# Optimization experiments

Hardware: AMD Instinct MI355X
Metric: run time of the kernel (lower is better)

The kernel has to match this reference:

```python
import jax, jax.numpy as jnp
import numpy as np

NUM_USERS = 50000
NUM_ITEMS = 20000
N_NODES = NUM_USERS + NUM_ITEMS
D = 128
CONTENT_DIM = 512
BATCH = 8192
N_EDGES = 500000
NEG_SLOPE = 0.2  # GATConv leaky_relu slope


def setup_inputs() -> dict:
    key = jax.random.key(0)
    ks = jax.random.split(key, 16)
    return {
        "user_ids": jax.random.randint(ks[0], (BATCH,), 0, NUM_USERS),
        "item_ids": jax.random.randint(ks[1], (BATCH,), 0, NUM_ITEMS),
        "content_features": jax.random.normal(ks[2], (BATCH, CONTENT_DIM), jnp.float32),
        "edge_index": jax.random.randint(ks[3], (2, N_EDGES), 0, N_NODES),
        "user_emb_w": jax.random.normal(ks[4], (NUM_USERS, D), jnp.float32) * 0.05,
        "item_emb_w": jax.random.normal(ks[5], (NUM_ITEMS, D), jnp.float32) * 0.05,
        "content_proj_w": jax.random.normal(ks[6], (D, CONTENT_DIM), jnp.float32) * 0.04,
        "content_proj_b": jnp.zeros((D,), jnp.float32),
        "conv1_lin_w": jax.random.normal(ks[7], (2 * D, 2 * D), jnp.float32) * 0.06,
        "conv1_att_src": jax.random.normal(ks[8], (2, D), jnp.float32) * 0.1,
        "conv1_att_dst": jax.random.normal(ks[9], (2, D), jnp.float32) * 0.1,
        "conv1_bias": jnp.zeros((2 * D,), jnp.float32),
        "conv2_lin_w": jax.random.normal(ks[10], (D, 2 * D), jnp.float32) * 0.06,
        "conv2_att_src": jax.random.normal(ks[11], (1, D), jnp.float32) * 0.1,
        "conv2_att_dst": jax.random.normal(ks[12], (1, D), jnp.float32) * 0.1,
        "conv2_bias": jnp.zeros((D,), jnp.float32),
        "pred_w1": jax.random.normal(ks[13], (D, 3 * D), jnp.float32) * 0.05,
        "pred_b1": jnp.zeros((D,), jnp.float32),
        "pred_w2": jax.random.normal(ks[14], (1, D), jnp.float32) * 0.09,
        "pred_b2": jnp.zeros((1,), jnp.float32),
    }


def gat_conv(x, src, dst, lin_w, att_src, att_dst, bias, heads, out_ch):
    # PyG GATConv (shared lin for src/dst, concat=True, add_self_loops handled outside)
    n = x.shape[0]
    h = (x @ lin_w.T).reshape(n, heads, out_ch)          # [N,H,C]
    a_src = jnp.sum(h * att_src, axis=-1)                # [N,H]
    a_dst = jnp.sum(h * att_dst, axis=-1)                # [N,H]
    alpha = jax.nn.leaky_relu(a_src[src] + a_dst[dst], NEG_SLOPE)  # [E,H]
    # softmax over incoming edges of each destination node
    amax = jax.ops.segment_max(alpha, dst, num_segments=n)
    ex = jnp.exp(alpha - amax[dst])
    denom = jax.ops.segment_sum(ex, dst, num_segments=n)
    w = ex / denom[dst]                                  # [E,H]
    out = jax.ops.segment_sum(h[src] * w[:, :, None], dst, num_segments=n)
    return out.reshape(n, heads * out_ch) + bias


def _forward(user_ids, item_ids, edge_index, content_features, user_emb_w, item_emb_w,
             content_proj_w, content_proj_b, conv1_lin_w, conv1_att_src, conv1_att_dst,
             conv1_bias, conv2_lin_w, conv2_att_src, conv2_att_dst, conv2_bias,
             pred_w1, pred_b1, pred_w2, pred_b2):
    u_emb = user_emb_w[user_ids]                         # [B,D]
    i_emb = item_emb_w[item_ids]                         # [B,D]
    c_emb = content_features @ content_proj_w.T + content_proj_b  # [B,D]
    # scatter-init sparse node features (only batch nodes are nonzero, as in source)
    x = jnp.zeros((N_NODES, 2 * D), jnp.float32)
    x = x.at[user_ids].set(jnp.concatenate([u_emb, jnp.zeros_like(c_emb)], axis=1))
    x = x.at[NUM_USERS + item_ids].set(jnp.concatenate([i_emb, c_emb], axis=1))
    # add self loops (fill_value irrelevant: edge_weight unused by GATConv)
    loops = jnp.arange(N_NODES, dtype=edge_index.dtype)
    src = jnp.concatenate([edge_index[0], loops])
    dst = jnp.concatenate([edge_index[1], loops])
    x = jax.nn.elu(gat_conv(x, src, dst, conv1_lin_w, conv1_att_src, conv1_att_dst, conv1_bias, 2, D))
    # dropout inactive (eval mode)
    x = gat_conv(x, src, dst, conv2_lin_w, conv2_att_src, conv2_att_dst, conv2_bias, 1, D)
    combined = jnp.concatenate([u_emb, x[NUM_USERS + item_ids], x[user_ids]], axis=1)  # [B,3D]
    h = jax.nn.relu(combined @ pred_w1.T + pred_b1)
    return (h @ pred_w2.T + pred_b2).squeeze(-1)         # [B]


def reference(user_ids, item_ids, content_features, edge_index, user_emb_w, item_emb_w,
              content_proj_w, content_proj_b, conv1_lin_w, conv1_att_src, conv1_att_dst,
              conv1_bias, conv2_lin_w, conv2_att_src, conv2_att_dst, conv2_bias,
              pred_w1, pred_b1, pred_w2, pred_b2):
    return _forward(user_ids, item_ids, edge_index, content_features, user_emb_w, item_emb_w,
                    content_proj_w, content_proj_b, conv1_lin_w, conv1_att_src, conv1_att_dst,
                    conv1_bias, conv2_lin_w, conv2_att_src, conv2_att_dst, conv2_bias,
                    pred_w1, pred_b1, pred_w2, pred_b2)
```

## Files before the change

### kernel.cpp

```cpp
#include <hip/hip_runtime.h>
#include <hip/hip_bf16.h>

#define NU 50000
#define NI 20000
#define NN 70000
#define DD 128
#define BB 8192
#define EE 500000
#define ET 570000
#define NTASK 16384

__device__ __forceinline__ float lrelu(float x) { return x > 0.f ? x : 0.2f * x; }

typedef __attribute__((ext_vector_type(8))) short bf16x8;
typedef __attribute__((ext_vector_type(8))) unsigned short u16x8;
typedef __attribute__((ext_vector_type(4))) float f32x4;

__device__ __forceinline__ unsigned short f2bf_rne(float f) {
  unsigned int u = __builtin_bit_cast(unsigned int, f);
  u += 0x7FFFu + ((u >> 16) & 1u);
  return (unsigned short)(u >> 16);
}
__device__ __forceinline__ float bf2f(unsigned short h) {
  unsigned int u = ((unsigned int)h) << 16;
  return __builtin_bit_cast(float, u);
}

__global__ __launch_bounds__(256) void clear_kernel(
    unsigned int* __restrict__ wsw,
    unsigned int offA, unsigned int nA,
    unsigned int offB, unsigned int nB,
    unsigned int offC, unsigned int nC,
    float* __restrict__ out) {
  unsigned int idx = blockIdx.x * 256 + threadIdx.x;
  unsigned int stride = gridDim.x * 256;
  for (unsigned int i = idx; i < nA; i += stride) wsw[offA + i] = 0xFFFFFFFFu;
  for (unsigned int i = idx; i < nB; i += stride) wsw[offB + i] = 0u;
  for (unsigned int i = idx; i < nC; i += stride) wsw[offC + i] = 0u;
  for (unsigned int i = idx; i < BB; i += stride) out[i] = 0.f;
}

template <int GATHER, int MODE>
__device__ __forceinline__ void gemm_core(
    int bm, int bn,
    const float* __restrict__ A,
    const unsigned short* __restrict__ Bh, const unsigned short* __restrict__ Bl,
    const float* __restrict__ bias, float* __restrict__ C,
    unsigned short* __restrict__ Cb, int ldc,
    int M, int N, int K, int act,
    const int* __restrict__ idx0, const int* __restrict__ idx1,
    const int* __restrict__ mapv,
    const float* __restrict__ gA0, const float* __restrict__ gA1,
    const float* __restrict__ att_s, const float* __restrict__ att_d,
    float* __restrict__ a1s, float* __restrict__ a1d) {
  __shared__ __align__(16) unsigned short sAh[8][64][8];
  __shared__ __align__(16) unsigned short sAl[8][64][8];
  __shared__ __align__(16) unsigned short sBh[8][64][8];
  __shared__ __align__(16) unsigned short sBl[8][64][8];
  int tid = threadIdx.x;
  int lane = tid & 63, w = tid >> 6;
  int wr = (w >> 1) * 32, wc = (w & 1) * 32;
  int fr = lane & 15, fk = lane >> 4;
  f32x4 acc[2][2] = {};

  for (int k0 = 0; k0 < K; k0 += 64) {
    __syncthreads();
#pragma unroll
    for (int t = 0; t < 2; t++) {
      int f = tid + t * 256;
      int row = f >> 3, kb = f & 7;
      int kg = k0 + kb * 8;
      const float* ap;
      if (GATHER == 1) {
        int sec = kg >> 7;
        int kc = kg & 127;
        int r = bm + row;
        if (sec == 0)      ap = &gA0[(size_t)idx0[r] * 128 + kc];
        else if (sec == 1) ap = &gA1[(size_t)mapv[NU + idx1[r]] * 128 + kc];
        else               ap = &gA1[(size_t)mapv[idx0[r]] * 128 + kc];
      } else if (GATHER == 2) {
        ap = &gA0[(size_t)idx0[bm + row] * K + kg];
      } else {
        ap = &A[(size_t)(bm + row) * K + kg];
      }
      float4 v0 = *reinterpret_cast<const float4*>(ap);
      float4 v1 = *reinterpret_cast<const float4*>(ap + 4);
      float vv[8] = {v0.x, v0.y, v0.z, v0.w, v1.x, v1.y, v1.z, v1.w};
      u16x8 hv, lv;
#pragma unroll
      for (int j = 0; j < 8; j++) {
        unsigned short hh = f2bf_rne(vv[j]);
        hv[j] = hh;
        lv[j] = (unsigned short)(__builtin_bit_cast(unsigned int, vv[j] - bf2f(hh)) >> 16);
      }
      *reinterpret_cast<u16x8*>(&sAh[kb][row][0]) = hv;
      *reinterpret_cast<u16x8*>(&sAl[kb][row][0]) = lv;
    }
#pragma unroll
    for (int t = 0; t < 2; t++) {
      int f = tid + t * 256;
      int row = f >> 3, kb = f & 7;
      int kg = k0 + kb * 8;
      *reinterpret_cast<u16x8*>(&sBh[kb][row][0]) =
          *reinterpret_cast<const u16x8*>(&Bh[(size_t)(bn + row) * K + kg]);
      *reinterpret_cast<u16x8*>(&sBl[kb][row][0]) =
          *reinterpret_cast<const u16x8*>(&Bl[(size_t)(bn + row) * K + kg]);
    }
    __syncthreads();
#pragma unroll
    for (int s = 0; s < 2; s++) {
      int kb = s * 4 + fk;
      bf16x8 ah0 = *reinterpret_cast<const bf16x8*>(&sAh[kb][wr + fr][0]);
      bf16x8 ah1 = *reinterpret_cast<const bf16x8*>(&sAh[kb][wr + 16 + fr][0]);
      bf16x8 al0 = *reinterpret_cast<const bf16x8*>(&sAl[kb][wr + fr][0]);
      bf16x8 al1 = *reinterpret_cast<const bf16x8*>(&sAl[kb][wr + 16 + fr][0]);
      bf16x8 bh0 = *reinterpret_cast<const bf16x8*>(&sBh[kb][wc + fr][0]);
      bf16x8 bh1 = *reinterpret_cast<const bf16x8*>(&sBh[kb][wc + 16 + fr][0]);
      bf16x8 bl0 = *reinterpret_cast<const bf16x8*>(&sBl[kb][wc + fr][0]);
      bf16x8 bl1 = *reinterpret_cast<const bf16x8*>(&sBl[kb][wc + 16 + fr][0]);
      acc[0][0] = __builtin_amdgcn_mfma_f32_16x16x32_bf16(al0, bh0, acc[0][0], 0, 0, 0);
      acc[0][0] = __builtin_amdgcn_mfma_f32_16x16x32_bf16(ah0, bl0, acc[0][0], 0, 0, 0);
      acc[0][0] = __builtin_amdgcn_mfma_f32_16x16x32_bf16(ah0, bh0, acc[0][0], 0, 0, 0);
      acc[0][1] = __builtin_amdgcn_mfma_f32_16x16x32_bf16(al0, bh1, acc[0][1], 0, 0, 0);
      acc[0][1] = __builtin_amdgcn_mfma_f32_16x16x32_bf16(ah0, bl1, acc[0][1], 0, 0, 0);
      acc[0][1] = __builtin_amdgcn_mfma_f32_16x16x32_bf16(ah0, bh1, acc[0][1], 0, 0, 0);
      acc[1][0] = __builtin_amdgcn_mfma_f32_16x16x32_bf16(al1, bh0, acc[1][0], 0, 0, 0);
      acc[1][0] = __builtin_amdgcn_mfma_f32_16x16x32_bf16(ah1, bl0, acc[1][0], 0, 0, 0);
      acc[1][0] = __builtin_amdgcn_mfma_f32_16x16x32_bf16(ah1, bh0, acc[1][0], 0, 0, 0);
      acc[1][1] = __builtin_amdgcn_mfma_f32_16x16x32_bf16(al1, bh1, acc[1][1], 0, 0, 0);
      acc[1][1] = __builtin_amdgcn_mfma_f32_16x16x32_bf16(ah1, bl1, acc[1][1], 0, 0, 0);
      acc[1][1] = __builtin_amdgcn_mfma_f32_16x16x32_bf16(ah1, bh1, acc[1][1], 0, 0, 0);
    }
  }
  if (MODE == 1) {
    int head = bn >> 7;
    float ps[2][4] = {{0.f}}, pd[2][4] = {{0.f}};
#pragma unroll
    for (int j = 0; j < 2; j++) {
      int col = bn + wc + j * 16 + fr;
      float asc = att_s[col], adc = att_d[col];
#pragma unroll
      for (int i = 0; i < 2; i++) {
#pragma unroll
        for (int r = 0; r < 4; r++) {
          float v = acc[i][j][r];
          ps[i][r] += v * asc;
          pd[i][r] += v * adc;
          Cb[(size_t)(bm + wr + i * 16 + fk * 4 + r) * ldc + col] = f2bf_rne(v);
        }
      }
    }
#pragma unroll
    for (int o = 1; o < 16; o <<= 1) {
#pragma unroll
      for (int i = 0; i < 2; i++)
#pragma unroll
        for (int r = 0; r < 4; r++) {
          ps[i][r] += __shfl_xor(ps[i][r], o);
          pd[i][r] += __shfl_xor(pd[i][r], o);
        }
    }
    if (fr == 0) {
#pragma unroll
      for (int i = 0; i < 2; i++) {
#pragma unroll
        for (int r = 0; r < 4; r++) {
          int t = bm + wr + i * 16 + fk * 4 + r;
          int v = (t < BB) ? idx0[t] : NU + idx1[t - BB];
          if (mapv[v] == t) {
            atomicAdd(&a1s[(size_t)v * 2 + head], ps[i][r]);
            atomicAdd(&a1d[(size_t)v * 2 + head], pd[i][r]);
          }
        }
      }
    }
    return;
  }
  if (MODE == 2) {
    float part[2][4] = {{0.f}};
#pragma unroll
    for (int j = 0; j < 2; j++) {
      int col = bn + wc + j * 16 + fr;
      float bj = bias[col];
      float wv = att_s[col];
#pragma unroll
      for (int i = 0; i < 2; i++) {
#pragma unroll
        for (int r = 0; r < 4; r++) {
          float v = fmaxf(acc[i][j][r] + bj, 0.f);
          part[i][r] += v * wv;
        }
      }
    }
#pragma unroll
    for (int o = 1; o < 16; o <<= 1) {
#pragma unroll
      for (int i = 0; i < 2; i++)
#pragma unroll
        for (int r = 0; r < 4; r++) part[i][r] += __shfl_xor(part[i][r], o);
    }
    if (fr == 0) {
#pragma unroll
      for (int i = 0; i < 2; i++) {
#pragma unroll
        for (int r = 0; r < 4; r++) {
          int row = bm + wr + i * 16 + fk * 4 + r;
          float add = part[i][r];
          if (bn == 0 && wc == 0) add += att_d[0];
          atomicAdd(&a1s[row], add);
        }
      }
    }
    return;
  }
#pragma unroll
  for (int j = 0; j < 2; j++) {
    int col = bn + wc + j * 16 + fr;
    float bj = bias ? bias[col] : 0.f;
#pragma unroll
    for (int i = 0; i < 2; i++) {
#pragma unroll
      for (int r = 0; r < 4; r++) {
        int row = bm + wr + i * 16 + fk * 4 + r;
        float v = acc[i][j][r] + bj;
        if (act == 1) v = fmaxf(v, 0.f);
        C[(size_t)row * ldc + col] = v;
      }
    }
  }
}

template <int GATHER, int MODE>
__global__ __launch_bounds__(256) void gemm_mfma(
    const float* __restrict__ A,
    const unsigned short* __restrict__ Bh, const unsigned short* __restrict__ Bl,
    const float* __restrict__ bias, float* __restrict__ C,
    unsigned short* __restrict__ Cb, int ldc,
    int M, int N, int K, int act,
    const int* __restrict__ idx0, const int* __restrict__ idx1,
    const int* __restrict__ mapv,
    const float* __restrict__ gA0, const float* __restrict__ gA1,
    const float* __restrict__ att_s, const float* __restrict__ att_d,
    float* __restrict__ a1s, float* __restrict__ a1d) {
  gemm_core<GATHER, MODE>(blockIdx.x * 64, blockIdx.y * 64,
                          A, Bh, Bl, bias, C, Cb, ldc, M, N, K, act,
                          idx0, idx1, mapv, gA0, gA1, att_s, att_d, a1s, a1d);
}

#define GEMMB 256
__global__ __launch_bounds__(256) void cembfill_kernel(
    const unsigned short* __restrict__ wch, const unsigned short* __restrict__ wcl,
    const float* __restrict__ bc, float* __restrict__ XaC,
    const int* __restrict__ widx, const float* __restrict__ content,
    const int* __restrict__ ei, int* __restrict__ fill, int* __restrict__ col,
    const int* __restrict__ mapv, unsigned char* __restrict__ needed) {
  int bid = blockIdx.x;
  if (bid < GEMMB) {
    gemm_core<2, 0>((bid >> 1) * 64, (bid & 1) * 64,
                    nullptr, wch, wcl, bc, XaC, nullptr, 256,
                    BB, DD, 512, 0, widx, nullptr, nullptr, content, nullptr,
                    nullptr, nullptr, nullptr, nullptr);
    return;
  }
  int e = (bid - GEMMB) * 256 + threadIdx.x;
  if (e >= ET) return;
  int src, dst;
  if (e < EE) { src = ei[e]; dst = ei[EE + e]; }
  else { src = e - EE; dst = src; }
  int pos = atomicAdd(&fill[dst], 1);
  col[pos] = src;
  if (mapv[dst] >= 0) needed[src] = 1;
}

#define EB 2227
#define SPLB 832
#define XAB 4096
__global__ __launch_bounds__(256) void setup_kernel(
    const int* __restrict__ ei, const int* __restrict__ uid, const int* __restrict__ iid,
    int* __restrict__ deg, int* __restrict__ winner,
    const float* __restrict__ wc, unsigned short* wch, unsigned short* wcl,
    const float* __restrict__ w1, unsigned short* w1h, unsigned short* w1l,
    const float* __restrict__ w2, unsigned short* w2h, unsigned short* w2l,
    const float* __restrict__ pw1, unsigned short* p1h, unsigned short* p1l,
    const float* __restrict__ uemb, const float* __restrict__ iemb,
    float* __restrict__ Xa, int* __restrict__ map) {
  int bid = blockIdx.x, tid = threadIdx.x;
  if (bid < EB) {
    int e = bid * 256 + tid;
    if (e < BB) atomicMax(&winner[iid[e]], e);
    if (e >= ET) return;
    int dst = (e < EE) ? ei[EE + e] : (e - EE);
    atomicAdd(&deg[dst], 1);
    return;
  }
  if (bid < EB + SPLB) {
    int i = (bid - EB) * 256 + tid;
    const float* w; unsigned short* h; unsigned short* l; int idx;
    if (i < 65536) { w = wc; h = wch; l = wcl; idx = i; }
    else if (i < 131072) { w = w1; h = w1h; l = w1l; idx = i - 65536; }
    else if (i < 163840) { w = w2; h = w2h; l = w2l; idx = i - 131072; }
    else { w = pw1; h = p1h; l = p1l; idx = i - 163840; }
    float f = w[idx];
    unsigned short hh = f2bf_rne(f);
    h[idx] = hh;
    l[idx] = (unsigned short)(__builtin_bit_cast(unsigned int, f - bf2f(hh)) >> 16);
    return;
  }
  int t = (bid - EB - SPLB) * 4 + (tid >> 6);
  int lane = tid & 63;
  int c4 = lane * 4;
  if (t < BB) {
    int u = uid[t];
    float4 v = make_float4(0.f, 0.f, 0.f, 0.f);
    if (c4 < DD) v = *reinterpret_cast<const float4*>(&uemb[(size_t)u * DD + c4]);
    *reinterpret_cast<float4*>(&Xa[(size_t)t * 256 + c4]) = v;
    if (lane == 0) map[u] = t;
  } else {
    int it = iid[t - BB];
    if (c4 < DD) {
      float4 v = *reinterpret_cast<const float4*>(&iemb[(size_t)it * DD + c4]);
      *reinterpret_cast<float4*>(&Xa[(size_t)t * 256 + c4]) = v;
    }
    if (lane == 0) map[NU + it] = t;
  }
}

__global__ void rowstart_kernel(const int* __restrict__ deg, const int* __restrict__ winner,
                                const int* __restrict__ iid,
                                int* __restrict__ rowstart, int* __restrict__ fill,
                                int* __restrict__ counter, int* __restrict__ widx,
                                const float* __restrict__ w2,
                                const float* __restrict__ att2s, const float* __restrict__ att2d,
                                float* __restrict__ qs, float* __restrict__ qd) {
  int blk = blockIdx.x;
  if (blk == (NN + 255) / 256) {
    int k = threadIdx.x;
    float s = 0.f, d = 0.f;
#pragma unroll 4
    for (int j = 0; j < DD; j++) {
      float w = w2[(size_t)j * 256 + k];
      s += att2s[j] * w;
      d += att2d[j] * w;
    }
    qs[k] = s;
    qd[k] = d;
    return;
  }
  int v = blk * 256 + threadIdx.x;
  if (v < BB) widx[v] = winner[iid[v]];
  int lane = threadIdx.x & 63;
  int dv = (v < NN) ? deg[v] : 0;
  int x = dv;
#pragma unroll
  for (int o = 1; o < 64; o <<= 1) {
    int y = __shfl_up(x, o);
    if (lane >= o) x += y;
  }
  int tot = __shfl(x, 63);
  int base = 0;
  if (lane == 63) base = atomicAdd(counter, tot);
  base = __shfl(base, 63);
  if (v < NN) {
    int s = base + x - dv;
    rowstart[v] = s;
    fill[v] = s;
  }
}

__global__ __launch_bounds__(256) void conv1_agg_kernel(
    const int* __restrict__ col, const int* __restrict__ rowstart,
    const int* __restrict__ deg, const unsigned short* __restrict__ Hb,
    const int* __restrict__ map, const unsigned char* __restrict__ needed,
    const float* __restrict__ a1s, const float* __restrict__ a1d,
    const float* __restrict__ bias,
    const float* __restrict__ qs, const float* __restrict__ qd,
    unsigned short* __restrict__ x1b, float* __restrict__ a2s, float* __restrict__ a2d) {
  int v = blockIdx.x * 4 + (threadIdx.x >> 6);
  int lane = threadIdx.x & 63;
  if (!needed[v]) return;
  int head = lane >> 5;
  int d = deg[v], s0 = rowstart[v];
  float2 adv = *reinterpret_cast<const float2*>(&a1d[(size_t)v * 2]);
  float4 acc = make_float4(0.f, 0.f, 0.f, 0.f);
  float den0 = 0.f, den1 = 0.f;
  const unsigned short* hb = Hb + (lane << 2);
  for (int c0 = 0; c0 < d; c0 += 64) {
    int i = c0 + lane;
    bool act = i < d;
    int ci = act ? col[s0 + i] : 0;
    float2 asv = make_float2(0.f, 0.f);
    int ri = -1;
    if (act) {
      asv = *reinterpret_cast<const float2*>(&a1s[(size_t)ci * 2]);
      ri = map[ci];
    }
    float ex0 = act ? __expf(lrelu(asv.x + adv.x)) : 0.f;
    float ex1 = act ? __expf(lrelu(asv.y + adv.y)) : 0.f;
    den0 += ex0;
    den1 += ex1;
    unsigned long long msk = __ballot(act && ri >= 0);
    while (msk) {
      int s = __ffsll((unsigned long long)msk) - 1;
      msk &= msk - 1;
      int r = __shfl(ri, s);
      float e0 = __shfl(ex0, s), e1 = __shfl(ex1, s);
      float ex = head ? e1 : e0;
      ushort4 hv = *reinterpret_cast<const ushort4*>(&hb[(size_t)r << 8]);
      acc.x += ex * bf2f(hv.x); acc.y += ex * bf2f(hv.y);
      acc.z += ex * bf2f(hv.z); acc.w += ex * bf2f(hv.w);
    }
  }
#pragma unroll
  for (int o = 1; o < 64; o <<= 1) {
    den0 += __shfl_xor(den0, o);
    den1 += __shfl_xor(den1, o);
  }
  float inv = 1.f / (head ? den1 : den0);
  float4 b4 = *reinterpret_cast<const float4*>(&bias[lane << 2]);
  float4 o;
  o.x = fmaf(acc.x, inv, b4.x);
  o.y = fmaf(acc.y, inv, b4.y);
  o.z = fmaf(acc.z, inv, b4.z);
  o.w = fmaf(acc.w, inv, b4.w);
  o.x = o.x > 0.f ? o.x : __expf(o.x) - 1.f;
  o.y = o.y > 0.f ? o.y : __expf(o.y) - 1.f;
  o.z = o.z > 0.f ? o.z : __expf(o.z) - 1.f;
  o.w = o.w > 0.f ? o.w : __expf(o.w) - 1.f;
  ushort4 st;
  st.x = f2bf_rne(o.x); st.y = f2bf_rne(o.y);
  st.z = f2bf_rne(o.z); st.w = f2bf_rne(o.w);
  *reinterpret_cast<ushort4*>(&x1b[((size_t)v << 8) + (lane << 2)]) = st;
  float4 sv = *reinterpret_cast<const float4*>(&qs[lane << 2]);
  float4 dv = *reinterpret_cast<const float4*>(&qd[lane << 2]);
  float ps = o.x * sv.x + o.y * sv.y + o.z * sv.z + o.w * sv.w;
  float pd = o.x * dv.x + o.y * dv.y + o.z * dv.z + o.w * dv.w;
#pragma unroll
  for (int of = 1; of < 64; of <<= 1) { ps += __shfl_xor(ps, of); pd += __shfl_xor(pd, of); }
  if (lane == 0) { a2s[v] = ps; a2d[v] = pd; }
}

__global__ __launch_bounds__(256) void conv2_agg_kernel(
    const int* __restrict__ uid, const int* __restrict__ iid,
    const int* __restrict__ col, const int* __restrict__ rowstart,
    const int* __restrict__ deg, const int* __restrict__ map,
    const unsigned short* __restrict__ x1b,
    const float* __restrict__ a2s, const float* __restrict__ a2d,
    float* __restrict__ agg) {
  int t = blockIdx.x * 4 + (threadIdx.x >> 6);
  int lane = threadIdx.x & 63;
  int v = (t < BB) ? uid[t] : NU + iid[t - BB];
  if (map[v] != t) return;
  int d = deg[v], s0 = rowstart[v];
  float ad = a2d[v];
  float4 acc = make_float4(0.f, 0.f, 0.f, 0.f);
  float den = 0.f;
  const unsigned short* xb = x1b + (lane << 2);
  for (int c0 = 0; c0 < d; c0 += 64) {
    int i = c0 + lane;
    bool act = i < d;
    int ci = act ? col[s0 + i] : 0;
    float as = act ? a2s[ci] : 0.f;
    float ex = act ? __expf(lrelu(as + ad)) : 0.f;
    den += ex;
    int n = min(64, d - c0);
#pragma unroll 2
    for (int i2 = 0; i2 < n; i2++) {
      int r = __shfl(ci, i2);
      float e = __shfl(ex, i2);
      ushort4 hv = *reinterpret_cast<const ushort4*>(&xb[(size_t)r << 8]);
      acc.x += e * bf2f(hv.x); acc.y += e * bf2f(hv.y);
      acc.z += e * bf2f(hv.z); acc.w += e * bf2f(hv.w);
    }
  }
#pragma unroll
  for (int o = 1; o < 64; o <<= 1) den += __shfl_xor(den, o);
  float inv = 1.f / den;
  float4 o = make_float4(acc.x * inv, acc.y * inv, acc.z * inv, acc.w * inv);
  *reinterpret_cast<float4*>(&agg[((size_t)t << 8) + (lane << 2)]) = o;
}

extern "C" void kernel_launch(void* const* d_in, const int* in_sizes, int n_in,
                              void* d_out, int out_size, void* d_ws, size_t ws_size,
                              hipStream_t stream) {
  const int* uid = (const int*)d_in[0];
  const int* iid = (const int*)d_in[1];
  const float* content = (const float*)d_in[2];
  const int* ei = (const int*)d_in[3];
  const float* uemb = (const float*)d_in[4];
  const float* iemb = (const float*)d_in[5];
  const float* wc = (const float*)d_in[6];
  const float* bc = (const float*)d_in[7];
  const float* w1 = (const float*)d_in[8];
  const float* att1s = (const float*)d_in[9];
  const float* att1d = (const float*)d_in[10];
  const float* b1 = (const float*)d_in[11];
  const float* w2 = (const float*)d_in[12];
  const float* att2s = (const float*)d_in[13];
  const float* att2d = (const float*)d_in[14];
  const float* b2c = (const float*)d_in[15];
  const float* pw1 = (const float*)d_in[16];
  const float* pb1 = (const float*)d_in[17];
  const float* pw2 = (const float*)d_in[18];
  const float* pb2 = (const float*)d_in[19];
  float* out = (float*)d_out;
  char* ws = (char*)d_ws;

  size_t off = 0;
  auto alloc = [&](size_t bytes) {
    size_t o = off;
    off += (bytes + 255) & ~(size_t)255;
    return o;
  };
  size_t o_winner  = alloc(NI * 4);
  size_t o_map     = alloc(NN * 4);
  size_t o_a1s     = alloc((size_t)NN * 2 * 4);
  size_t o_a1d     = alloc((size_t)NN * 2 * 4);
  size_t o_deg     = alloc(NN * 4);
  size_t o_rs      = alloc(NN * 4);
  size_t o_fill    = alloc(NN * 4);
  size_t o_cnt     = alloc(4);
  size_t o_needed  = alloc(NN);
  size_t o_col     = alloc((size_t)ET * 4);
  size_t o_a2s     = alloc(NN * 4);
  size_t o_a2d     = alloc(NN * 4);
  size_t o_qs      = alloc(256 * 4);
  size_t o_qd      = alloc(256 * 4);
  size_t o_widx    = alloc(BB * 4);
  size_t o_wch = alloc(65536 * 2),  o_wcl = alloc(65536 * 2);
  size_t o_w1h = alloc(65536 * 2),  o_w1l = alloc(65536 * 2);
  size_t o_w2h = alloc(32768 * 2),  o_w2l = alloc(32768 * 2);
  size_t o_p1h = alloc(49152 * 2),  o_p1l = alloc(49152 * 2);
  size_t o_r1    = alloc(16777216 + 8388608);
  size_t o_xa    = o_r1;
  size_t o_hb    = o_r1 + 16777216;
  size_t o_agg   = o_r1;
  size_t o_out2c = o_r1 + 16777216;
  size_t o_x1b   = alloc((size_t)NN * 256 * 2);
  (void)ws_size; (void)in_sizes; (void)n_in; (void)out_size;

  int*   winner = (int*)(ws + o_winner);
  int*   map    = (int*)(ws + o_map);
  float* a1s    = (float*)(ws + o_a1s);
  float* a1d    = (float*)(ws + o_a1d);
  int*   deg    = (int*)(ws + o_deg);
  int*   rs     = (int*)(ws + o_rs);
  int*   fill   = (int*)(ws + o_fill);
  int*   cnt    = (int*)(ws + o_cnt);
  unsigned char* needed = (unsigned char*)(ws + o_needed);
  int*   col    = (int*)(ws + o_col);
  float* a2s    = (float*)(ws + o_a2s);
  float* a2d    = (float*)(ws + o_a2d);
  float* qs     = (float*)(ws + o_qs);
  float* qd     = (float*)(ws + o_qd);
  int*   widx   = (int*)(ws + o_widx);
  unsigned short* wch = (unsigned short*)(ws + o_wch);
  unsigned short* wcl = (unsigned short*)(ws + o_wcl);
  unsigned short* w1h = (unsigned short*)(ws + o_w1h);
  unsigned short* w1l = (unsigned short*)(ws + o_w1l);
  unsigned short* w2h = (unsigned short*)(ws + o_w2h);
  unsigned short* w2l = (unsigned short*)(ws + o_w2l);
  unsigned short* p1h = (unsigned short*)(ws + o_p1h);
  unsigned short* p1l = (unsigned short*)(ws + o_p1l);
  float* Xa     = (float*)(ws + o_xa);
  unsigned short* Hb = (unsigned short*)(ws + o_hb);
  float* agg    = (float*)(ws + o_agg);
  float* out2c  = (float*)(ws + o_out2c);
  unsigned short* x1b = (unsigned short*)(ws + o_x1b);

  {
    unsigned int offA = (unsigned int)(o_winner >> 2);
    unsigned int nA   = (unsigned int)((o_map - o_winner) / 4 + NN);
    unsigned int offB = (unsigned int)(o_a1s >> 2);
    unsigned int nB   = (unsigned int)((o_a1d - o_a1s) / 4 + (size_t)NN * 2);
    unsigned int offC = (unsigned int)(o_deg >> 2);
    unsigned int nC   = (unsigned int)((o_needed - o_deg) / 4 + NN / 4);
    clear_kernel<<<1024, 256, 0, stream>>>((unsigned int*)ws, offA, nA, offB, nB,
                                           offC, nC, out);
  }

  setup_kernel<<<EB + SPLB + XAB, 256, 0, stream>>>(
      ei, uid, iid, deg, winner,
      wc, wch, wcl, w1, w1h, w1l, w2, w2h, w2l, pw1, p1h, p1l,
      uemb, iemb, Xa, map);
  rowstart_kernel<<<(NN + 255) / 256 + 1, 256, 0, stream>>>(
      deg, winner, iid, rs, fill, cnt, widx, w2, att2s, att2d, qs, qd);
  cembfill_kernel<<<GEMMB + EB, 256, 0, stream>>>(
      wch, wcl, bc, Xa + (size_t)BB * 256 + 128, widx, content,
      ei, fill, col, map, needed);
  {
    dim3 g(NTASK / 64, 256 / 64);
    gemm_mfma<0, 1><<<g, 256, 0, stream>>>(
        Xa, w1h, w1l, nullptr, nullptr, Hb, 256,
        NTASK, 256, 256, 0, uid, iid, map, nullptr, nullptr,
        att1s, att1d, a1s, a1d);
  }
  conv1_agg_kernel<<<NN / 4, 256, 0, stream>>>(col, rs, deg, Hb, map, needed,
                                               a1s, a1d, b1, qs, qd, x1b, a2s, a2d);
  conv2_agg_kernel<<<NTASK / 4, 256, 0, stream>>>(uid, iid, col, rs, deg, map,
                                                  x1b, a2s, a2d, agg);
  {
    dim3 g(NTASK / 64, DD / 64);
    gemm_mfma<0, 0><<<g, 256, 0, stream>>>(
        agg, w2h, w2l, b2c, out2c, nullptr, 128,
        NTASK, DD, 256, 0, nullptr, nullptr, nullptr, nullptr, nullptr,
        nullptr, nullptr, nullptr, nullptr);
  }
  {
    dim3 g(BB / 64, DD / 64);
    gemm_mfma<1, 2><<<g, 256, 0, stream>>>(
        nullptr, p1h, p1l, pb1, nullptr, nullptr, 128,
        BB, DD, 384, 0, uid, iid, map, uemb, out2c,
        pw2, pb2, out, nullptr);
  }
}
```

Measured before the change: 196.1 us.

## Merge rowstart with content GEMM and edge fill with conv1 GEMM launches

Moves the content-projection GEMM into the rowstart scan kernel, reading winner[iid] directly through a new gather mode instead of a precomputed widx array. The CSR edge fill is then merged with the conv1 linear GEMM into one launch. This cuts one kernel launch and lets independent work overlap within each launch. It relies on the conv1 GEMM reading Xa columns produced by the content GEMM in the previous launch, which stays correct because the two kernels run in stream order.

```diff
diff --git a/kernel.cpp b/kernel.cpp
--- a/kernel.cpp
+++ b/kernel.cpp
@@ -80,6 +80,8 @@
         else               ap = &gA1[(size_t)mapv[idx0[r]] * 128 + kc];
       } else if (GATHER == 2) {
         ap = &gA0[(size_t)idx0[bm + row] * K + kg];
+      } else if (GATHER == 3) {
+        ap = &gA0[(size_t)mapv[idx0[bm + row]] * K + kg];
       } else {
         ap = &A[(size_t)(bm + row) * K + kg];
       }
@@ -247,31 +249,6 @@
                           idx0, idx1, mapv, gA0, gA1, att_s, att_d, a1s, a1d);
 }
 
-#define GEMMB 256
-__global__ __launch_bounds__(256) void cembfill_kernel(
-    const unsigned short* __restrict__ wch, const unsigned short* __restrict__ wcl,
-    const float* __restrict__ bc, float* __restrict__ XaC,
-    const int* __restrict__ widx, const float* __restrict__ content,
-    const int* __restrict__ ei, int* __restrict__ fill, int* __restrict__ col,
-    const int* __restrict__ mapv, unsigned char* __restrict__ needed) {
-  int bid = blockIdx.x;
-  if (bid < GEMMB) {
-    gemm_core<2, 0>((bid >> 1) * 64, (bid & 1) * 64,
-                    nullptr, wch, wcl, bc, XaC, nullptr, 256,
-                    BB, DD, 512, 0, widx, nullptr, nullptr, content, nullptr,
-                    nullptr, nullptr, nullptr, nullptr);
-    return;
-  }
-  int e = (bid - GEMMB) * 256 + threadIdx.x;
-  if (e >= ET) return;
-  int src, dst;
-  if (e < EE) { src = ei[e]; dst = ei[EE + e]; }
-  else { src = e - EE; dst = src; }
-  int pos = atomicAdd(&fill[dst], 1);
-  col[pos] = src;
-  if (mapv[dst] >= 0) needed[src] = 1;
-}
-
 #define EB 2227
 #define SPLB 832
 #define XAB 4096
@@ -325,15 +302,41 @@
   }
 }
 
-__global__ void rowstart_kernel(const int* __restrict__ deg, const int* __restrict__ winner,
-                                const int* __restrict__ iid,
-                                int* __restrict__ rowstart, int* __restrict__ fill,
-                                int* __restrict__ counter, int* __restrict__ widx,
-                                const float* __restrict__ w2,
-                                const float* __restrict__ att2s, const float* __restrict__ att2d,
-                                float* __restrict__ qs, float* __restrict__ qd) {
+#define RSB 274
+#define CEMBB 256
+__global__ __launch_bounds__(256) void rowcemb_kernel(
+    const int* __restrict__ deg,
+    int* __restrict__ rowstart, int* __restrict__ fill, int* __restrict__ counter,
+    const float* __restrict__ w2,
+    const float* __restrict__ att2s, const float* __restrict__ att2d,
+    float* __restrict__ qs, float* __restrict__ qd,
+    const unsigned short* __restrict__ wch, const unsigned short* __restrict__ wcl,
+    const float* __restrict__ bc, float* __restrict__ XaC,
+    const int* __restrict__ iid, const int* __restrict__ winner,
+    const float* __restrict__ content) {
   int blk = blockIdx.x;
-  if (blk == (NN + 255) / 256) {
+  if (blk < RSB) {
+    int v = blk * 256 + threadIdx.x;
+    int lane = threadIdx.x & 63;
+    int dv = (v < NN) ? deg[v] : 0;
+    int x = dv;
+#pragma unroll
+    for (int o = 1; o < 64; o <<= 1) {
+      int y = __shfl_up(x, o);
+      if (lane >= o) x += y;
+    }
+    int tot = __shfl(x, 63);
+    int base = 0;
+    if (lane == 63) base = atomicAdd(counter, tot);
+    base = __shfl(base, 63);
+    if (v < NN) {
+      int s = base + x - dv;
+      rowstart[v] = s;
+      fill[v] = s;
+    }
+    return;
+  }
+  if (blk == RSB) {
     int k = threadIdx.x;
     float s = 0.f, d = 0.f;
 #pragma unroll 4
@@ -346,25 +349,40 @@
     qd[k] = d;
     return;
   }
-  int v = blk * 256 + threadIdx.x;
-  if (v < BB) widx[v] = winner[iid[v]];
-  int lane = threadIdx.x & 63;
-  int dv = (v < NN) ? deg[v] : 0;
-  int x = dv;
-#pragma unroll
-  for (int o = 1; o < 64; o <<= 1) {
-    int y = __shfl_up(x, o);
-    if (lane >= o) x += y;
-  }
-  int tot = __shfl(x, 63);
-  int base = 0;
-  if (lane == 63) base = atomicAdd(counter, tot);
-  base = __shfl(base, 63);
-  if (v < NN) {
-    int s = base + x - dv;
-    rowstart[v] = s;
-    fill[v] = s;
-  }
+  int t = blk - RSB - 1;
+  gemm_core<3, 0>((t >> 1) * 64, (t & 1) * 64,
+                  nullptr, wch, wcl, bc, XaC, nullptr, 256,
+                  BB, DD, 512, 0, iid, nullptr, winner, content, nullptr,
+                  nullptr, nullptr, nullptr, nullptr);
+}
+
+#define HBB 1024
+__global__ __launch_bounds__(256) void fillhb_kernel(
+    const int* __restrict__ ei, int* __restrict__ fill, int* __restrict__ col,
+    const int* __restrict__ mapv, unsigned char* __restrict__ needed,
+    const float* __restrict__ Xa,
+    const unsigned short* __restrict__ w1h, const unsigned short* __restrict__ w1l,
+    unsigned short* __restrict__ Hb,
+    const int* __restrict__ uid, const int* __restrict__ iid,
+    const float* __restrict__ att1s, const float* __restrict__ att1d,
+    float* __restrict__ a1s, float* __restrict__ a1d) {
+  int bid = blockIdx.x;
+  if (bid < EB) {
+    int e = bid * 256 + threadIdx.x;
+    if (e >= ET) return;
+    int src, dst;
+    if (e < EE) { src = ei[e]; dst = ei[EE + e]; }
+    else { src = e - EE; dst = src; }
+    int pos = atomicAdd(&fill[dst], 1);
+    col[pos] = src;
+    if (mapv[dst] >= 0) needed[src] = 1;
+    return;
+  }
+  int t = bid - EB;
+  gemm_core<0, 1>((t >> 2) * 64, (t & 3) * 64,
+                  Xa, w1h, w1l, nullptr, nullptr, Hb, 256,
+                  NTASK, 256, 256, 0, uid, iid, mapv, nullptr, nullptr,
+                  att1s, att1d, a1s, a1d);
 }
 
 __global__ __launch_bounds__(256) void conv1_agg_kernel(
@@ -525,7 +543,6 @@
   size_t o_a2d     = alloc(NN * 4);
   size_t o_qs      = alloc(256 * 4);
   size_t o_qd      = alloc(256 * 4);
-  size_t o_widx    = alloc(BB * 4);
   size_t o_wch = alloc(65536 * 2),  o_wcl = alloc(65536 * 2);
   size_t o_w1h = alloc(65536 * 2),  o_w1l = alloc(65536 * 2);
   size_t o_w2h = alloc(32768 * 2),  o_w2l = alloc(32768 * 2);
@@ -552,7 +569,6 @@
   float* a2d    = (float*)(ws + o_a2d);
   float* qs     = (float*)(ws + o_qs);
   float* qd     = (float*)(ws + o_qd);
-  int*   widx   = (int*)(ws + o_widx);
   unsigned short* wch = (unsigned short*)(ws + o_wch);
   unsigned short* wcl = (unsigned short*)(ws + o_wcl);
   unsigned short* w1h = (unsigned short*)(ws + o_w1h);
@@ -582,18 +598,12 @@
       ei, uid, iid, deg, winner,
       wc, wch, wcl, w1, w1h, w1l, w2, w2h, w2l, pw1, p1h, p1l,
       uemb, iemb, Xa, map);
-  rowstart_kernel<<<(NN + 255) / 256 + 1, 256, 0, stream>>>(
-      deg, winner, iid, rs, fill, cnt, widx, w2, att2s, att2d, qs, qd);
-  cembfill_kernel<<<GEMMB + EB, 256, 0, stream>>>(
-      wch, wcl, bc, Xa + (size_t)BB * 256 + 128, widx, content,
-      ei, fill, col, map, needed);
-  {
-    dim3 g(NTASK / 64, 256 / 64);
-    gemm_mfma<0, 1><<<g, 256, 0, stream>>>(
-        Xa, w1h, w1l, nullptr, nullptr, Hb, 256,
-        NTASK, 256, 256, 0, uid, iid, map, nullptr, nullptr,
-        att1s, att1d, a1s, a1d);
-  }
+  rowcemb_kernel<<<RSB + 1 + CEMBB, 256, 0, stream>>>(
+      deg, rs, fill, cnt, w2, att2s, att2d, qs, qd,
+      wch, wcl, bc, Xa + (size_t)BB * 256 + 128, iid, winner, content);
+  fillhb_kernel<<<EB + HBB, 256, 0, stream>>>(
+      ei, fill, col, map, needed, Xa, w1h, w1l, Hb,
+      uid, iid, att1s, att1d, a1s, a1d);
   conv1_agg_kernel<<<NN / 4, 256, 0, stream>>>(col, rs, deg, Hb, map, needed,
                                                a1s, a1d, b1, qs, qd, x1b, a2s, a2d);
   conv2_agg_kernel<<<NTASK / 4, 256, 0, stream>>>(uid, iid, col, rs, deg, map,
```

Result: no change. 195.0 us (-0.6%).
